# Performance work log

Hardware: AMD Instinct MI355X
Metric: run time of the kernel (lower is better)

## Reference

```python
import jax, jax.numpy as jnp
import numpy as np

HEADS = 8

def _proj(x, W, b):
    # 1x1 conv == per-pixel linear: x [B,C,H,W], W [O,C], b [O]
    return jnp.einsum('bchw,oc->bohw', x, W) + b[None, :, None, None]

def setup_inputs() -> dict:
    key = jax.random.key(0)
    ks = jax.random.split(key, 9)
    B, C, H, W = 8, 256, 32, 32
    s = C ** -0.5
    return {
        'x':  jax.random.normal(ks[0], (B, C, H, W), jnp.float32),
        'Wq': jax.random.normal(ks[1], (C, C), jnp.float32) * s,
        'bq': jax.random.normal(ks[2], (C,), jnp.float32) * 0.02,
        'Wk': jax.random.normal(ks[3], (C, C), jnp.float32) * s,
        'bk': jax.random.normal(ks[4], (C,), jnp.float32) * 0.02,
        'Wv': jax.random.normal(ks[5], (C, C), jnp.float32) * s,
        'bv': jax.random.normal(ks[6], (C,), jnp.float32) * 0.02,
        'Wm': jax.random.normal(ks[7], (C, C), jnp.float32) * s,
        'bm': jax.random.normal(ks[8], (C,), jnp.float32) * 0.02,
    }

def reference(x, Wq, bq, Wk, bk, Wv, bv, Wm, bm):
    B, C, H, W = x.shape
    h = HEADS
    hd = C // h
    scale = hd ** -0.5

    def to_heads(t):
        # [B,C,H,W] -> [B,h,hd,H,W] -> [B,h,HW,hd]
        t = t.reshape(B, h, hd, H, W)
        return t.transpose(0, 1, 3, 4, 2).reshape(B, h, H * W, hd)

    q = to_heads(_proj(x, Wq, bq))
    k = to_heads(_proj(x, Wk, bk))
    v = to_heads(_proj(x, Wv, bv))

    attn = jax.nn.softmax(jnp.einsum('bhnd,bhmd->bhnm', q, k) * scale, axis=-1)
    out = jnp.einsum('bhnm,bhmd->bhnd', attn, v)          # [B,h,HW,hd]
    # torch: view(B,h,H,W,hd).permute(0,4,1,2,3).view(B,C,H,W) => channel = d*h + head
    out = out.reshape(B, h, H, W, hd).transpose(0, 4, 1, 2, 3).reshape(B, C, H, W)
    return _proj(out, Wm, bm)
```

## Files before the change

kernel.cpp:

```cpp
#include <hip/hip_runtime.h>
#include <cstdint>
#include <cstddef>


#define NB 8
#define NC 256
#define NP 1024
#define NHD 8
#define HD 32

typedef short bf16x8 __attribute__((ext_vector_type(8)));
typedef float f32x4 __attribute__((ext_vector_type(4)));

#define SCLLOG 0.25505654356918f

__device__ __forceinline__ unsigned cvt_pk_bf16(float a, float b) {
  unsigned r;
  asm("v_cvt_pk_bf16_f32 %0, %1, %2" : "=v"(r) : "v"(a), "v"(b));
  return r;
}
__device__ __forceinline__ unsigned short f2b1(float a) {
  return (unsigned short)cvt_pk_bf16(a, a);
}

__global__ __launch_bounds__(256) void prep_kernel(
    const float* __restrict__ Wq, const float* __restrict__ Wk,
    const float* __restrict__ Wv, const float* __restrict__ Wm,
    const float* __restrict__ x, unsigned short* __restrict__ Wb,
    unsigned short* __restrict__ xt) {
  __shared__ float sx[64][65];
  int bx = blockIdx.x, tid = threadIdx.x;
  if (bx < 128) {
    int idx = (bx * 256 + tid) * 8;
    const float* src; int off;
    if (idx < 65536)       { src = Wq; off = idx; }
    else if (idx < 131072) { src = Wk; off = idx - 65536; }
    else if (idx < 196608) { src = Wv; off = idx - 131072; }
    else                   { src = Wm; off = idx - 196608; }
    float4 lo = *(const float4*)(src + off);
    float4 hi = *(const float4*)(src + off + 4);
    union { unsigned u[4]; bf16x8 v; } o;
    o.u[0] = cvt_pk_bf16(lo.x, lo.y); o.u[1] = cvt_pk_bf16(lo.z, lo.w);
    o.u[2] = cvt_pk_bf16(hi.x, hi.y); o.u[3] = cvt_pk_bf16(hi.z, hi.w);
    *(bf16x8*)(Wb + idx) = o.v;
  } else {
    int bi = bx - 128;
    int b = bi >> 6, rest = bi & 63;
    int ct = (rest & 3) * 64, pt = (rest >> 2) * 64;
    const float* xb = x + ((size_t)(b * NC + ct)) * NP + pt;
    int pr = (tid & 15) * 4, cr = tid >> 4;
#pragma unroll
    for (int i = 0; i < 4; i++) {
      float4 v = *(const float4*)(xb + (size_t)(cr + i * 16) * NP + pr);
      sx[cr + i*16][pr]   = v.x; sx[cr + i*16][pr+1] = v.y;
      sx[cr + i*16][pr+2] = v.z; sx[cr + i*16][pr+3] = v.w;
    }
    __syncthreads();
    int pl = tid >> 3, cc = (tid & 7) * 8;
#pragma unroll
    for (int j = 0; j < 2; j++) {
      int p = pl + j * 32;
      union { unsigned u[4]; bf16x8 v; } o;
#pragma unroll
      for (int u = 0; u < 4; u++)
        o.u[u] = cvt_pk_bf16(sx[cc + 2*u][p], sx[cc + 2*u + 1][p]);
      *(bf16x8*)(xt + ((size_t)b * NP + pt + p) * NC + ct + cc) = o.v;
    }
  }
}

__global__ __launch_bounds__(256) void qkv_kernel(
    const unsigned short* __restrict__ Wb,
    const float* __restrict__ bq, const float* __restrict__ bk,
    const float* __restrict__ bv,
    const unsigned short* __restrict__ xt,
    unsigned short* __restrict__ qt, unsigned short* __restrict__ kt,
    unsigned short* __restrict__ vt) {
  int proj = blockIdx.z, b = blockIdx.y, bx = blockIdx.x;
  int ot = (bx & 3) * 64, pt = (bx >> 2) * 64;
  int tid = threadIdx.x, wave = tid >> 6, lane = tid & 63;
  int l15 = lane & 15, quad = lane >> 4;
  int oW = ot + (wave & 1) * 32, pW = pt + (wave >> 1) * 32;
  const unsigned short* W = Wb + (size_t)proj * 65536;
  const float* bias = (proj == 0) ? bq : (proj == 1) ? bk : bv;
  const unsigned short* A0 = W + (size_t)(oW + l15) * NC + quad * 8;
  const unsigned short* B0 = xt + ((size_t)b * NP + pW + l15) * NC + quad * 8;
  f32x4 acc[2][2];
#pragma unroll
  for (int i = 0; i < 2; i++)
#pragma unroll
    for (int j = 0; j < 2; j++) acc[i][j] = (f32x4){0.f, 0.f, 0.f, 0.f};
#pragma unroll
  for (int c0 = 0; c0 < NC; c0 += 32) {
    bf16x8 a0 = *(const bf16x8*)(A0 + c0);
    bf16x8 a1 = *(const bf16x8*)(A0 + 16 * NC + c0);
    bf16x8 b0 = *(const bf16x8*)(B0 + c0);
    bf16x8 b1 = *(const bf16x8*)(B0 + 16 * NC + c0);
    acc[0][0] = __builtin_amdgcn_mfma_f32_16x16x32_bf16(a0, b0, acc[0][0], 0, 0, 0);
    acc[0][1] = __builtin_amdgcn_mfma_f32_16x16x32_bf16(a0, b1, acc[0][1], 0, 0, 0);
    acc[1][0] = __builtin_amdgcn_mfma_f32_16x16x32_bf16(a1, b0, acc[1][0], 0, 0, 0);
    acc[1][1] = __builtin_amdgcn_mfma_f32_16x16x32_bf16(a1, b1, acc[1][1], 0, 0, 0);
  }
  unsigned short* qk = (proj == 0) ? qt : kt;
#pragma unroll
  for (int rh = 0; rh < 2; rh++) {
    int od0 = oW + rh * 16 + quad * 4;
    float b0 = bias[od0], b1 = bias[od0+1], b2 = bias[od0+2], b3 = bias[od0+3];
#pragma unroll
    for (int ch = 0; ch < 2; ch++) {
      float v0 = acc[rh][ch][0] + b0, v1 = acc[rh][ch][1] + b1;
      float v2 = acc[rh][ch][2] + b2, v3 = acc[rh][ch][3] + b3;
      if (proj < 2) {
        int p = pW + ch * 16 + l15;
        int h2 = od0 >> 5, d0 = od0 & 31;
        uint2 pk;
        pk.x = cvt_pk_bf16(v0, v1);
        pk.y = cvt_pk_bf16(v2, v3);
        size_t idx = ((size_t)(b * NHD + h2) * NP + p) * HD + d0;
        *(uint2*)(qk + idx) = pk;
      } else {
        int p2 = pW + 2 * l15 + ch;
        size_t base = ((size_t)b * NC + od0) * NP + p2;
        vt[base]          = f2b1(v0);
        vt[base +     NP] = f2b1(v1);
        vt[base + 2 * NP] = f2b1(v2);
        vt[base + 3 * NP] = f2b1(v3);
      }
    }
  }
}

__global__ __launch_bounds__(256) void attn_kernel(
    const unsigned short* __restrict__ qt, const unsigned short* __restrict__ kt,
    const unsigned short* __restrict__ vt, unsigned short* __restrict__ at) {
  int tid = threadIdx.x, wave = tid >> 6, lane = tid & 63;
  int l15 = lane & 15, quad = lane >> 4;
  int bh = blockIdx.y, b = bh >> 3, h = bh & 7;
  int n0 = blockIdx.x * 128 + wave * 32;
  __shared__ __align__(16) unsigned short P[4][1280];
  unsigned short* Pw = &P[wave][0];

  bf16x8 qfa = *(const bf16x8*)(qt + ((size_t)bh * NP + n0 + l15) * HD + quad * 8);
  bf16x8 qfb = *(const bf16x8*)(qt + ((size_t)bh * NP + n0 + 16 + l15) * HD + quad * 8);
  const unsigned short* kp = kt + (size_t)bh * NP * HD + (size_t)l15 * HD + quad * 8;
  const unsigned short* vp = vt + ((size_t)(b * NC + h * HD) + l15) * NP + quad * 8;

  union { unsigned u[4]; bf16x8 v; } ones;
  ones.u[0] = ones.u[1] = ones.u[2] = ones.u[3] = 0x3F803F80u;

  f32x4 oa0 = (f32x4){0.f,0.f,0.f,0.f}, oa1 = (f32x4){0.f,0.f,0.f,0.f};
  f32x4 ob0 = (f32x4){0.f,0.f,0.f,0.f}, ob1 = (f32x4){0.f,0.f,0.f,0.f};
  f32x4 la  = (f32x4){0.f,0.f,0.f,0.f}, lb  = (f32x4){0.f,0.f,0.f,0.f};
  const f32x4 z = (f32x4){0.f,0.f,0.f,0.f};

  bf16x8 kf0 = *(const bf16x8*)(kp);
  bf16x8 kf1 = *(const bf16x8*)(kp + 16 * HD);
  bf16x8 vf0 = *(const bf16x8*)(vp);
  bf16x8 vf1 = *(const bf16x8*)(vp + 16 * NP);

  for (int m0 = 0; m0 < NP; m0 += 32) {
    f32x4 s0a = __builtin_amdgcn_mfma_f32_16x16x32_bf16(qfa, kf0, z, 0, 0, 0);
    f32x4 s1a = __builtin_amdgcn_mfma_f32_16x16x32_bf16(qfa, kf1, z, 0, 0, 0);
    f32x4 s0b = __builtin_amdgcn_mfma_f32_16x16x32_bf16(qfb, kf0, z, 0, 0, 0);
    f32x4 s1b = __builtin_amdgcn_mfma_f32_16x16x32_bf16(qfb, kf1, z, 0, 0, 0);
    bf16x8 nk0 = *(const bf16x8*)(kp + (m0 + 32) * HD);
    bf16x8 nk1 = *(const bf16x8*)(kp + (m0 + 48) * HD);
    bf16x8 nv0 = *(const bf16x8*)(vp + m0 + 32);
    bf16x8 nv1 = *(const bf16x8*)(vp + 16 * NP + m0 + 32);
#pragma unroll
    for (int r = 0; r < 4; r++) {
      float pa0 = __builtin_amdgcn_exp2f(fmaf(s0a[r], SCLLOG, -16.0f));
      float pa1 = __builtin_amdgcn_exp2f(fmaf(s1a[r], SCLLOG, -16.0f));
      float pb0 = __builtin_amdgcn_exp2f(fmaf(s0b[r], SCLLOG, -16.0f));
      float pb1 = __builtin_amdgcn_exp2f(fmaf(s1b[r], SCLLOG, -16.0f));
      *(unsigned*)(Pw + (quad * 4 + r) * 40 + 2 * l15)       = cvt_pk_bf16(pa0, pa1);
      *(unsigned*)(Pw + 640 + (quad * 4 + r) * 40 + 2 * l15) = cvt_pk_bf16(pb0, pb1);
    }
    bf16x8 pfa = *(const bf16x8*)(Pw + l15 * 40 + quad * 8);
    bf16x8 pfb = *(const bf16x8*)(Pw + 640 + l15 * 40 + quad * 8);
    oa0 = __builtin_amdgcn_mfma_f32_16x16x32_bf16(pfa, vf0, oa0, 0, 0, 0);
    oa1 = __builtin_amdgcn_mfma_f32_16x16x32_bf16(pfa, vf1, oa1, 0, 0, 0);
    ob0 = __builtin_amdgcn_mfma_f32_16x16x32_bf16(pfb, vf0, ob0, 0, 0, 0);
    ob1 = __builtin_amdgcn_mfma_f32_16x16x32_bf16(pfb, vf1, ob1, 0, 0, 0);
    la  = __builtin_amdgcn_mfma_f32_16x16x32_bf16(pfa, ones.v, la, 0, 0, 0);
    lb  = __builtin_amdgcn_mfma_f32_16x16x32_bf16(pfb, ones.v, lb, 0, 0, 0);
    kf0 = nk0; kf1 = nk1; vf0 = nv0; vf1 = nv1;
  }
  unsigned short* ab = at + (size_t)b * NP * NC;
#pragma unroll
  for (int r = 0; r < 4; r++) {
    float inva = 1.0f / la[r], invb = 1.0f / lb[r];
    int na = n0 + quad * 4 + r, nb = n0 + 16 + quad * 4 + r;
    ab[(size_t)na * NC + (l15 * 8 + h)]        = f2b1(oa0[r] * inva);
    ab[(size_t)na * NC + ((16 + l15) * 8 + h)] = f2b1(oa1[r] * inva);
    ab[(size_t)nb * NC + (l15 * 8 + h)]        = f2b1(ob0[r] * invb);
    ab[(size_t)nb * NC + ((16 + l15) * 8 + h)] = f2b1(ob1[r] * invb);
  }
}

__global__ __launch_bounds__(256) void mproj_kernel(
    const unsigned short* __restrict__ Wmb, const float* __restrict__ bm,
    const unsigned short* __restrict__ at, float* __restrict__ out) {
  int b = blockIdx.y, bx = blockIdx.x;
  int ot = (bx & 3) * 64, pt = (bx >> 2) * 64;
  int tid = threadIdx.x, wave = tid >> 6, lane = tid & 63;
  int l15 = lane & 15, quad = lane >> 4;
  int oW = ot + (wave & 1) * 32, pW = pt + (wave >> 1) * 32;
  const unsigned short* A0 = Wmb + (size_t)(oW + l15) * NC + quad * 8;
  const unsigned short* B0 = at + ((size_t)b * NP + pW + l15) * NC + quad * 8;
  f32x4 acc[2][2];
#pragma unroll
  for (int i = 0; i < 2; i++)
#pragma unroll
    for (int j = 0; j < 2; j++) acc[i][j] = (f32x4){0.f, 0.f, 0.f, 0.f};
#pragma unroll
  for (int c0 = 0; c0 < NC; c0 += 32) {
    bf16x8 a0 = *(const bf16x8*)(A0 + c0);
    bf16x8 a1 = *(const bf16x8*)(A0 + 16 * NC + c0);
    bf16x8 b0 = *(const bf16x8*)(B0 + c0);
    bf16x8 b1 = *(const bf16x8*)(B0 + 16 * NC + c0);
    acc[0][0] = __builtin_amdgcn_mfma_f32_16x16x32_bf16(a0, b0, acc[0][0], 0, 0, 0);
    acc[0][1] = __builtin_amdgcn_mfma_f32_16x16x32_bf16(a0, b1, acc[0][1], 0, 0, 0);
    acc[1][0] = __builtin_amdgcn_mfma_f32_16x16x32_bf16(a1, b0, acc[1][0], 0, 0, 0);
    acc[1][1] = __builtin_amdgcn_mfma_f32_16x16x32_bf16(a1, b1, acc[1][1], 0, 0, 0);
  }
#pragma unroll
  for (int rh = 0; rh < 2; rh++) {
    int od0 = oW + rh * 16 + quad * 4;
    float b0 = bm[od0], b1 = bm[od0+1], b2 = bm[od0+2], b3 = bm[od0+3];
#pragma unroll
    for (int ch = 0; ch < 2; ch++) {
      int p = pW + ch * 16 + l15;
      size_t base = ((size_t)b * NC + od0) * NP + p;
      out[base]          = acc[rh][ch][0] + b0;
      out[base +     NP] = acc[rh][ch][1] + b1;
      out[base + 2 * NP] = acc[rh][ch][2] + b2;
      out[base + 3 * NP] = acc[rh][ch][3] + b3;
    }
  }
}

extern "C" void kernel_launch(void* const* d_in, const int* in_sizes, int n_in,
                              void* d_out, int out_size, void* d_ws, size_t ws_size,
                              hipStream_t stream) {
  (void)in_sizes; (void)n_in; (void)out_size; (void)ws_size;
  const float* x  = (const float*)d_in[0];
  const float* Wq = (const float*)d_in[1];
  const float* bq = (const float*)d_in[2];
  const float* Wk = (const float*)d_in[3];
  const float* bk = (const float*)d_in[4];
  const float* Wv = (const float*)d_in[5];
  const float* bv = (const float*)d_in[6];
  const float* Wm = (const float*)d_in[7];
  const float* bm = (const float*)d_in[8];
  float* out = (float*)d_out;
  char* ws = (char*)d_ws;

  unsigned short* xt = (unsigned short*)(ws);
  unsigned short* Wb = (unsigned short*)(ws + (4u << 20));
  unsigned short* qt = (unsigned short*)(ws + (4u << 20) + (512u << 10));
  unsigned short* kt = (unsigned short*)(ws + (8u << 20) + (512u << 10));
  unsigned short* vt = (unsigned short*)(ws + (12u << 20) + (512u << 10));
  unsigned short* at = (unsigned short*)(ws + (16u << 20) + (512u << 10));

  prep_kernel<<<640, 256, 0, stream>>>(Wq, Wk, Wv, Wm, x, Wb, xt);
  qkv_kernel<<<dim3(64, 8, 3), 256, 0, stream>>>(Wb, bq, bk, bv, xt, qt, kt, vt);
  attn_kernel<<<dim3(8, 64), 256, 0, stream>>>(qt, kt, vt, at);
  mproj_kernel<<<dim3(64, 8), 256, 0, stream>>>(Wb + 3 * 65536, bm, at, out);
}
```

Before: 138.2 us.

## Split attention key range across two wave groups and combine via LDS

The attention block grows to 512 threads. Each group of four waves processes half of the key/value sequence for the same 128 queries. Because the softmax uses a fixed max offset, the partial numerators and denominators can simply be added: the second half writes its accumulators to shared memory and the first half sums them and writes the output. This doubles the waves in flight per block to hide latency, at the cost of extra LDS, one block barrier and possibly lower block residency.

Result: no change. 137.0 us (-0.8%).

```diff
diff --git a/kernel.cpp b/kernel.cpp
--- a/kernel.cpp
+++ b/kernel.cpp
@@ -130,14 +130,16 @@
   }
 }
 
-__global__ __launch_bounds__(256) void attn_kernel(
+__global__ __launch_bounds__(512) void attn_kernel(
     const unsigned short* __restrict__ qt, const unsigned short* __restrict__ kt,
     const unsigned short* __restrict__ vt, unsigned short* __restrict__ at) {
   int tid = threadIdx.x, wave = tid >> 6, lane = tid & 63;
   int l15 = lane & 15, quad = lane >> 4;
+  int half = wave >> 2, wsub = wave & 3;
   int bh = blockIdx.y, b = bh >> 3, h = bh & 7;
-  int n0 = blockIdx.x * 128 + wave * 32;
-  __shared__ __align__(16) unsigned short P[4][1280];
+  int n0 = blockIdx.x * 128 + wsub * 32;
+  __shared__ __align__(16) unsigned short P[8][1280];
+  __shared__ float Comb[4][64][25];
   unsigned short* Pw = &P[wave][0];
 
   bf16x8 qfa = *(const bf16x8*)(qt + ((size_t)bh * NP + n0 + l15) * HD + quad * 8);
@@ -153,12 +155,13 @@
   f32x4 la  = (f32x4){0.f,0.f,0.f,0.f}, lb  = (f32x4){0.f,0.f,0.f,0.f};
   const f32x4 z = (f32x4){0.f,0.f,0.f,0.f};
 
-  bf16x8 kf0 = *(const bf16x8*)(kp);
-  bf16x8 kf1 = *(const bf16x8*)(kp + 16 * HD);
-  bf16x8 vf0 = *(const bf16x8*)(vp);
-  bf16x8 vf1 = *(const bf16x8*)(vp + 16 * NP);
-
-  for (int m0 = 0; m0 < NP; m0 += 32) {
+  int mbase = half * 512;
+  bf16x8 kf0 = *(const bf16x8*)(kp + mbase * HD);
+  bf16x8 kf1 = *(const bf16x8*)(kp + (mbase + 16) * HD);
+  bf16x8 vf0 = *(const bf16x8*)(vp + mbase);
+  bf16x8 vf1 = *(const bf16x8*)(vp + 16 * NP + mbase);
+
+  for (int m0 = mbase; m0 < mbase + 512; m0 += 32) {
     f32x4 s0a = __builtin_amdgcn_mfma_f32_16x16x32_bf16(qfa, kf0, z, 0, 0, 0);
     f32x4 s1a = __builtin_amdgcn_mfma_f32_16x16x32_bf16(qfa, kf1, z, 0, 0, 0);
     f32x4 s0b = __builtin_amdgcn_mfma_f32_16x16x32_bf16(qfb, kf0, z, 0, 0, 0);
@@ -186,15 +189,35 @@
     lb  = __builtin_amdgcn_mfma_f32_16x16x32_bf16(pfb, ones.v, lb, 0, 0, 0);
     kf0 = nk0; kf1 = nk1; vf0 = nv0; vf1 = nv1;
   }
-  unsigned short* ab = at + (size_t)b * NP * NC;
-#pragma unroll
-  for (int r = 0; r < 4; r++) {
-    float inva = 1.0f / la[r], invb = 1.0f / lb[r];
-    int na = n0 + quad * 4 + r, nb = n0 + 16 + quad * 4 + r;
-    ab[(size_t)na * NC + (l15 * 8 + h)]        = f2b1(oa0[r] * inva);
-    ab[(size_t)na * NC + ((16 + l15) * 8 + h)] = f2b1(oa1[r] * inva);
-    ab[(size_t)nb * NC + (l15 * 8 + h)]        = f2b1(ob0[r] * invb);
-    ab[(size_t)nb * NC + ((16 + l15) * 8 + h)] = f2b1(ob1[r] * invb);
+
+  if (half == 1) {
+    float* C = &Comb[wsub][lane][0];
+#pragma unroll
+    for (int r = 0; r < 4; r++) {
+      C[r]      = oa0[r];  C[4 + r]  = oa1[r];
+      C[8 + r]  = ob0[r];  C[12 + r] = ob1[r];
+      C[16 + r] = la[r];   C[20 + r] = lb[r];
+    }
+  }
+  __syncthreads();
+  if (half == 0) {
+    const float* C = &Comb[wsub][lane][0];
+#pragma unroll
+    for (int r = 0; r < 4; r++) {
+      oa0[r] += C[r];      oa1[r] += C[4 + r];
+      ob0[r] += C[8 + r];  ob1[r] += C[12 + r];
+      la[r]  += C[16 + r]; lb[r]  += C[20 + r];
+    }
+    unsigned short* ab = at + (size_t)b * NP * NC;
+#pragma unroll
+    for (int r = 0; r < 4; r++) {
+      float inva = 1.0f / la[r], invb = 1.0f / lb[r];
+      int na = n0 + quad * 4 + r, nb = n0 + 16 + quad * 4 + r;
+      ab[(size_t)na * NC + (l15 * 8 + h)]        = f2b1(oa0[r] * inva);
+      ab[(size_t)na * NC + ((16 + l15) * 8 + h)] = f2b1(oa1[r] * inva);
+      ab[(size_t)nb * NC + (l15 * 8 + h)]        = f2b1(ob0[r] * invb);
+      ab[(size_t)nb * NC + ((16 + l15) * 8 + h)] = f2b1(ob1[r] * invb);
+    }
   }
 }
 
@@ -265,6 +288,6 @@
 
   prep_kernel<<<640, 256, 0, stream>>>(Wq, Wk, Wv, Wm, x, Wb, xt);
   qkv_kernel<<<dim3(64, 8, 3), 256, 0, stream>>>(Wb, bq, bk, bv, xt, qt, kt, vt);
-  attn_kernel<<<dim3(8, 64), 256, 0, stream>>>(qt, kt, vt, at);
+  attn_kernel<<<dim3(8, 64), 512, 0, stream>>>(qt, kt, vt, at);
   mproj_kernel<<<dim3(64, 8), 256, 0, stream>>>(Wb + 3 * 65536, bm, at, out);
 }
```
